# Optimization experiments

Measured on AMD Instinct MI355X. Metric: run time of the kernel, lower is better.

## Reference

```python
import jax, jax.numpy as jnp
import numpy as np

LAMBDA_GEO = 0.5


def setup_inputs() -> dict:
    key = jax.random.key(0)
    embeddings = jax.random.normal(key, (4, 2048, 512), dtype=jnp.float32)
    return {"embeddings": embeddings}


def _geometric_loss(embeddings):
    b, s, d = embeddings.shape
    x = embeddings.reshape(b * s, d)  # [N, d]
    sq_norm = jnp.sum(x * x, axis=-1)  # [N]
    sq = sq_norm[:, None] + sq_norm[None, :] - 2.0 * (x @ x.T)  # [N, N]
    sq = jnp.maximum(sq, 0.0)
    dist = jnp.sqrt(sq)  # torch.cdist(p=2)
    return jnp.mean(jnp.exp(-dist * 0.1)) * 0.1


def reference(embeddings):
    geometric_loss = _geometric_loss(embeddings)
    total_geometric = LAMBDA_GEO * geometric_loss
    return geometric_loss, total_geometric
```

## Files before the change

### kernel.cpp

```cpp
#include <hip/hip_runtime.h>

#define NROWS 8192
#define DIM   512
#define NT    64
#define NTRI  (NT * (NT + 1) / 2)
#define NACC  64

using f32x4 = __attribute__((ext_vector_type(4))) float;

typedef __attribute__((address_space(1))) const void* as1_cvptr;
typedef __attribute__((address_space(3))) void*       as3_vptr;

__device__ __forceinline__ void async16(const void* g, void* l) {
    __builtin_amdgcn_global_load_lds((as1_cvptr)g, (as3_vptr)l, 16, 0, 0);
}

__device__ __forceinline__ unsigned char f2e4m3(float x) {
    unsigned ux = __float_as_uint(x);
    unsigned s  = (ux >> 24) & 0x80u;
    float a = __uint_as_float(ux & 0x7FFFFFFFu);
    a = fminf(a, 448.0f);
    unsigned ua = __float_as_uint(a);
    int eb = (int)(ua >> 23);
    if (eb < 121) eb = 121;
    float step  = __uint_as_float((unsigned)(eb - 3) << 23);
    float istep = __uint_as_float((unsigned)(257 - eb) << 23);
    float q = rintf(a * istep) * step;
    q = fminf(q, 448.0f);
    if (q < 0.001953125f)
        return (unsigned char)s;
    unsigned uq = __float_as_uint(q);
    int eq = (int)(uq >> 23) - 127;
    unsigned byte;
    if (eq < -6) byte = (unsigned)(q * 512.0f);
    else         byte = (unsigned)((eq + 7) << 3) | ((uq >> 20) & 7u);
    return (unsigned char)(s | byte);
}

__global__ __launch_bounds__(256) void norm_convert_kernel(
    const float* __restrict__ X, unsigned char* __restrict__ Xq,
    float* __restrict__ norms, float* __restrict__ acc)
{
    const int tid  = threadIdx.x;
    const int lane = tid & 63;
    const int w    = tid >> 6;
    const int row  = blockIdx.x * 4 + w;

    if (blockIdx.x == 0 && tid < NACC) acc[tid] = 0.0f;

    const float* xr = X + (size_t)row * DIM + lane * 8;
    float4 v0 = *(const float4*)xr;
    float4 v1 = *(const float4*)(xr + 4);

    float s = 0.0f;
    s = fmaf(v0.x, v0.x, s); s = fmaf(v0.y, v0.y, s);
    s = fmaf(v0.z, v0.z, s); s = fmaf(v0.w, v0.w, s);
    s = fmaf(v1.x, v1.x, s); s = fmaf(v1.y, v1.y, s);
    s = fmaf(v1.z, v1.z, s); s = fmaf(v1.w, v1.w, s);

    union { unsigned char b[8]; uint2 v; } pk;
    pk.b[0] = f2e4m3(v0.x); pk.b[1] = f2e4m3(v0.y);
    pk.b[2] = f2e4m3(v0.z); pk.b[3] = f2e4m3(v0.w);
    pk.b[4] = f2e4m3(v1.x); pk.b[5] = f2e4m3(v1.y);
    pk.b[6] = f2e4m3(v1.z); pk.b[7] = f2e4m3(v1.w);

    const int slab = lane >> 3;
    const int cpos = (lane & 7) ^ ((row >> 1) & 7);
    *(uint2*)(Xq + (size_t)row * DIM + slab * 64 + cpos * 8) = pk.v;

    #pragma unroll
    for (int off = 32; off > 0; off >>= 1) s += __shfl_down(s, off, 64);
    if (lane == 0) norms[row] = s;
}

__global__ __launch_bounds__(256, 4) void pair_loss_gemm_kernel(
    const unsigned char* __restrict__ Xq, const float* __restrict__ norms,
    float* __restrict__ acc)
{
    __shared__ __align__(16) char As0[8192];
    __shared__ __align__(16) char As1[8192];
    __shared__ __align__(16) char Bs0[8192];
    __shared__ __align__(16) char Bs1[8192];
    __shared__ float wsum[4];

    int t = blockIdx.x, bi = 0;
    while (t >= (NT - bi)) { t -= (NT - bi); bi++; }
    const int bj = bi + t;

    const int tid  = threadIdx.x;
    const int lane = tid & 63;
    const int w    = tid >> 6;

    const int rowA = bi * 128;
    const int rowB = bj * 128;

    f32x4 accv[4][4];
    const f32x4 zero = {0.0f, 0.0f, 0.0f, 0.0f};
    #pragma unroll
    for (int a = 0; a < 4; a++)
        #pragma unroll
        for (int b = 0; b < 4; b++) accv[a][b] = zero;

    const int i0 = w * 128 + lane;
    const int rr = i0 >> 2;
    const int sl = i0 & 3;
    const unsigned char* gAl = Xq + (size_t)(rowA + rr) * DIM + sl * 16;
    const unsigned char* gBl = Xq + (size_t)(rowB + rr) * DIM + sl * 16;
    const int ldw = w * 2048;

    const int fr  = lane & 15;
    const int q   = lane >> 4;
    const int fo0 = fr * 64 + ((q ^ ((fr >> 1) & 7)) * 8);
    const int wr  = (w & 1) * 64;
    const int wc  = (w >> 1) * 64;

    async16(gAl,        As0 + ldw);
    async16(gAl + 8192, As0 + ldw + 1024);
    async16(gBl,        Bs0 + ldw);
    async16(gBl + 8192, Bs0 + ldw + 1024);
    __syncthreads();

    char* curA = As0; char* nxtA = As1;
    char* curB = Bs0; char* nxtB = Bs1;

    #pragma unroll 1
    for (int k = 0; k < 8; k++) {
        long afr[2][4], bfr[2][4];
        #pragma unroll
        for (int s = 0; s < 2; s++) {
            const int fo = fo0 ^ (s << 5);
            #pragma unroll
            for (int a = 0; a < 4; a++)
                afr[s][a] = *(const long*)(curA + (wr + a * 16) * 64 + fo);
            #pragma unroll
            for (int b = 0; b < 4; b++)
                bfr[s][b] = *(const long*)(curB + (wc + b * 16) * 64 + fo);
        }

        const bool more = (k < 7);
        if (more) {
            const int k0 = (k + 1) * 64;
            async16(gAl + k0,        nxtA + ldw);
            async16(gAl + k0 + 8192, nxtA + ldw + 1024);
            async16(gBl + k0,        nxtB + ldw);
            async16(gBl + k0 + 8192, nxtB + ldw + 1024);
        }

        #pragma unroll
        for (int s = 0; s < 2; s++)
            #pragma unroll
            for (int a = 0; a < 4; a++)
                #pragma unroll
                for (int b = 0; b < 4; b++)
                    accv[a][b] = __builtin_amdgcn_mfma_f32_16x16x32_fp8_fp8(
                        afr[s][a], bfr[s][b], accv[a][b], 0, 0, 0);

        if (more) {
            __syncthreads();
            char* tA = curA; curA = nxtA; nxtA = tA;
            char* tB = curB; curB = nxtB; nxtB = tB;
        }
    }

    const float wgt = (bi == bj) ? 1.0f : 2.0f;
    float lsum = 0.0f;
    #pragma unroll
    for (int a = 0; a < 4; a++) {
        const int gi0 = rowA + wr + a * 16 + (lane >> 4) * 4;
        #pragma unroll
        for (int b = 0; b < 4; b++) {
            const int gj = rowB + wc + b * 16 + (lane & 15);
            const float nj = norms[gj];
            #pragma unroll
            for (int r = 0; r < 4; r++) {
                const int gi = gi0 + r;
                float sq = fmaf(-2.0f, accv[a][b][r], norms[gi] + nj);
                sq = fmaxf(sq, 0.0f);
                float term = __expf(-0.1f * sqrtf(sq));
                if (gi == gj) term = 1.0f;
                lsum += term;
            }
        }
    }
    lsum *= wgt;
    #pragma unroll
    for (int off = 32; off > 0; off >>= 1) lsum += __shfl_down(lsum, off, 64);
    if (lane == 0) wsum[w] = lsum;
    __syncthreads();
    if (tid == 0)
        atomicAdd(&acc[blockIdx.x & (NACC - 1)],
                  wsum[0] + wsum[1] + wsum[2] + wsum[3]);
}

__global__ void finalize_kernel(const float* __restrict__ acc,
                                float* __restrict__ out)
{
    const int lane = threadIdx.x;
    float s = (lane < NACC) ? acc[lane] : 0.0f;
    #pragma unroll
    for (int off = 32; off > 0; off >>= 1) s += __shfl_down(s, off, 64);
    if (lane == 0) {
        const float inv = 1.0f / ((float)NROWS * (float)NROWS);
        float loss = s * inv * 0.1f;
        out[0] = loss;
        out[1] = 0.5f * loss;
    }
}

extern "C" void kernel_launch(void* const* d_in, const int* in_sizes, int n_in,
                              void* d_out, int out_size, void* d_ws, size_t ws_size,
                              hipStream_t stream)
{
    const float* X = (const float*)d_in[0];
    float* out = (float*)d_out;

    char* ws = (char*)d_ws;
    float*         acc   = (float*)ws;
    float*         norms = (float*)(ws + 1024);
    unsigned char* Xq    = (unsigned char*)(ws + 1024 + 32768);

    norm_convert_kernel<<<NROWS / 4, 256, 0, stream>>>(X, Xq, norms, acc);
    pair_loss_gemm_kernel<<<NTRI, 256, 0, stream>>>(Xq, norms, acc);
    finalize_kernel<<<1, 64, 0, stream>>>(acc, out);
}
```

Baseline: 105.2 us.

## Use 128x256 block tiles with 512 threads and strict-upper-triangle masking

The pairwise GEMM block tile grows from 128x128 to 128x256 columns, run by 8 waves instead of 4. The triangular enumeration changes to row tiles of 128 against column tiles of 256, giving 1056 blocks. Each block stages one A tile shared across twice as many B columns, which cuts A reloads and per-block overhead. Diagonal handling now counts only pairs with gj > gi (weighted by 2) and adds the N diagonal ones analytically in finalize. The cost is wasted MFMA work on tiles that straddle the diagonal, plus higher LDS use per block (48KB), which may limit occupancy.

```diff
diff --git a/kernel.cpp b/kernel.cpp
--- a/kernel.cpp
+++ b/kernel.cpp
@@ -3,7 +3,8 @@
 #define NROWS 8192
 #define DIM   512
 #define NT    64
-#define NTRI  (NT * (NT + 1) / 2)
+#define NJT   32
+#define NBLK  1056
 #define NACC  64
 
 using f32x4 = __attribute__((ext_vector_type(4))) float;
@@ -73,26 +74,24 @@
     if (lane == 0) norms[row] = s;
 }
 
-__global__ __launch_bounds__(256, 4) void pair_loss_gemm_kernel(
+__global__ __launch_bounds__(512, 4) void pair_loss_gemm_kernel(
     const unsigned char* __restrict__ Xq, const float* __restrict__ norms,
     float* __restrict__ acc)
 {
-    __shared__ __align__(16) char As0[8192];
-    __shared__ __align__(16) char As1[8192];
-    __shared__ __align__(16) char Bs0[8192];
-    __shared__ __align__(16) char Bs1[8192];
-    __shared__ float wsum[4];
+    __shared__ __align__(16) char As[2][8192];
+    __shared__ __align__(16) char Bs[2][16384];
+    __shared__ float wsum[8];
 
     int t = blockIdx.x, bi = 0;
-    while (t >= (NT - bi)) { t -= (NT - bi); bi++; }
-    const int bj = bi + t;
+    while (t >= (NJT - (bi >> 1))) { t -= (NJT - (bi >> 1)); bi++; }
+    const int J = (bi >> 1) + t;
 
     const int tid  = threadIdx.x;
     const int lane = tid & 63;
     const int w    = tid >> 6;
 
     const int rowA = bi * 128;
-    const int rowB = bj * 128;
+    const int colB = J * 256;
 
     f32x4 accv[4][4];
     const f32x4 zero = {0.0f, 0.0f, 0.0f, 0.0f};
@@ -101,12 +100,15 @@
         #pragma unroll
         for (int b = 0; b < 4; b++) accv[a][b] = zero;
 
-    const int i0 = w * 128 + lane;
-    const int rr = i0 >> 2;
-    const int sl = i0 & 3;
-    const unsigned char* gAl = Xq + (size_t)(rowA + rr) * DIM + sl * 16;
-    const unsigned char* gBl = Xq + (size_t)(rowB + rr) * DIM + sl * 16;
-    const int ldw = w * 2048;
+    const int ciA = w * 64 + lane;
+    const unsigned char* gA =
+        Xq + (size_t)(rowA + (ciA >> 2)) * DIM + (ciA & 3) * 16;
+    const int ciB0 = w * 128 + lane;
+    const unsigned char* gB0 =
+        Xq + (size_t)(colB + (ciB0 >> 2)) * DIM + (ciB0 & 3) * 16;
+    const unsigned char* gB1 = gB0 + (size_t)16 * DIM;
+    const int lA = w * 1024;
+    const int lB = w * 2048;
 
     const int fr  = lane & 15;
     const int q   = lane >> 4;
@@ -114,17 +116,17 @@
     const int wr  = (w & 1) * 64;
     const int wc  = (w >> 1) * 64;
 
-    async16(gAl,        As0 + ldw);
-    async16(gAl + 8192, As0 + ldw + 1024);
-    async16(gBl,        Bs0 + ldw);
-    async16(gBl + 8192, Bs0 + ldw + 1024);
+    async16(gA,  As[0] + lA);
+    async16(gB0, Bs[0] + lB);
+    async16(gB1, Bs[0] + lB + 1024);
     __syncthreads();
-
-    char* curA = As0; char* nxtA = As1;
-    char* curB = Bs0; char* nxtB = Bs1;
 
     #pragma unroll 1
     for (int k = 0; k < 8; k++) {
+        const int cur = k & 1;
+        const char* curA = As[cur];
+        const char* curB = Bs[cur];
+
         long afr[2][4], bfr[2][4];
         #pragma unroll
         for (int s = 0; s < 2; s++) {
@@ -139,11 +141,11 @@
 
         const bool more = (k < 7);
         if (more) {
-            const int k0 = (k + 1) * 64;
-            async16(gAl + k0,        nxtA + ldw);
-            async16(gAl + k0 + 8192, nxtA + ldw + 1024);
-            async16(gBl + k0,        nxtB + ldw);
-            async16(gBl + k0 + 8192, nxtB + ldw + 1024);
+            const int nxt = cur ^ 1;
+            const int k0  = (k + 1) * 64;
+            async16(gA  + k0, As[nxt] + lA);
+            async16(gB0 + k0, Bs[nxt] + lB);
+            async16(gB1 + k0, Bs[nxt] + lB + 1024);
         }
 
         #pragma unroll
@@ -155,21 +157,16 @@
                     accv[a][b] = __builtin_amdgcn_mfma_f32_16x16x32_fp8_fp8(
                         afr[s][a], bfr[s][b], accv[a][b], 0, 0, 0);
 
-        if (more) {
-            __syncthreads();
-            char* tA = curA; curA = nxtA; nxtA = tA;
-            char* tB = curB; curB = nxtB; nxtB = tB;
-        }
-    }
-
-    const float wgt = (bi == bj) ? 1.0f : 2.0f;
+        if (more) __syncthreads();
+    }
+
     float lsum = 0.0f;
     #pragma unroll
     for (int a = 0; a < 4; a++) {
-        const int gi0 = rowA + wr + a * 16 + (lane >> 4) * 4;
+        const int gi0 = rowA + wr + a * 16 + q * 4;
         #pragma unroll
         for (int b = 0; b < 4; b++) {
-            const int gj = rowB + wc + b * 16 + (lane & 15);
+            const int gj = colB + wc + b * 16 + fr;
             const float nj = norms[gj];
             #pragma unroll
             for (int r = 0; r < 4; r++) {
@@ -177,19 +174,20 @@
                 float sq = fmaf(-2.0f, accv[a][b][r], norms[gi] + nj);
                 sq = fmaxf(sq, 0.0f);
                 float term = __expf(-0.1f * sqrtf(sq));
-                if (gi == gj) term = 1.0f;
-                lsum += term;
+                lsum += (gj > gi) ? 2.0f * term : 0.0f;
             }
         }
     }
-    lsum *= wgt;
     #pragma unroll
     for (int off = 32; off > 0; off >>= 1) lsum += __shfl_down(lsum, off, 64);
     if (lane == 0) wsum[w] = lsum;
     __syncthreads();
-    if (tid == 0)
-        atomicAdd(&acc[blockIdx.x & (NACC - 1)],
-                  wsum[0] + wsum[1] + wsum[2] + wsum[3]);
+    if (tid == 0) {
+        float bsum = 0.0f;
+        #pragma unroll
+        for (int i = 0; i < 8; i++) bsum += wsum[i];
+        atomicAdd(&acc[blockIdx.x & (NACC - 1)], bsum);
+    }
 }
 
 __global__ void finalize_kernel(const float* __restrict__ acc,
@@ -201,7 +199,7 @@
     for (int off = 32; off > 0; off >>= 1) s += __shfl_down(s, off, 64);
     if (lane == 0) {
         const float inv = 1.0f / ((float)NROWS * (float)NROWS);
-        float loss = s * inv * 0.1f;
+        float loss = (s + 8192.0f) * inv * 0.1f;
         out[0] = loss;
         out[1] = 0.5f * loss;
     }
@@ -220,6 +218,6 @@
     unsigned char* Xq    = (unsigned char*)(ws + 1024 + 32768);
 
     norm_convert_kernel<<<NROWS / 4, 256, 0, stream>>>(X, Xq, norms, acc);
-    pair_loss_gemm_kernel<<<NTRI, 256, 0, stream>>>(Xq, norms, acc);
+    pair_loss_gemm_kernel<<<NBLK, 512, 0, stream>>>(Xq, norms, acc);
     finalize_kernel<<<1, 64, 0, stream>>>(acc, out);
 }
```

After: 112.8 us. 7.2% more time.
